# Kernel tuning notes

Measured on AMD Instinct MI355X. Metric: run time of the kernel, lower is better.

## Reference

```python
import jax, jax.numpy as jnp
import numpy as np

DEPTH = 3
N = 32768          # total nodes
G = 256            # num graphs
P = N // G         # nodes per graph (last node is the virtual node)
E = 524288         # edges
IN, H, H2 = 8, 64, 128


def _lin(key, out_d, in_d):
    w = jax.random.normal(key, (out_d, in_d), dtype=jnp.float32) * (1.0 / np.sqrt(in_d))
    b = jnp.zeros((out_d,), dtype=jnp.float32)
    return w, b


def setup_inputs() -> dict:
    key = jax.random.key(0)
    ks = jax.random.split(key, 10)
    x = jax.random.normal(ks[0], (N, IN), dtype=jnp.float32)
    edge_index = jax.random.randint(ks[1], (2, E), 0, N, dtype=jnp.int32).astype(jnp.int64)
    batch = (jnp.arange(N, dtype=jnp.int64) // P)
    W1, b1 = _lin(ks[2], H, IN)
    W2, b2 = _lin(ks[3], H, H)
    W3, b3 = _lin(ks[4], H, H)
    W4, b4 = _lin(ks[5], H, 2 * H)
    W5, b5 = _lin(ks[6], H, H * H)
    Wd1, bd1 = _lin(ks[7], H2, H)
    Wd2, bd2 = _lin(ks[8], 1, H2)
    return {"x": x, "edge_index": edge_index, "batch": batch, "num_graphs": G,
            "W1": W1, "b1": b1, "W2": W2, "b2": b2, "W3": W3, "b3": b3,
            "W4": W4, "b4": b4, "W5": W5, "b5": b5,
            "Wd1": Wd1, "bd1": bd1, "Wd2": Wd2, "bd2": bd2}


def reference(x, edge_index, batch, num_graphs,
              W1, b1, W2, b2, W3, b3, W4, b4, W5, b5, Wd1, bd1, Wd2, bd2):
    # initial embed: linear -> relu -> L2 normalize
    h = jax.nn.relu(x @ W1.T + b1)
    h = h / jnp.linalg.norm(h, axis=-1, keepdims=True)
    src, dst = edge_index[0], edge_index[1]
    for _ in range(DEPTH):
        # sum-aggregate neighbor messages (PyG add aggregation: gather src, scatter-add to dst)
        m = jax.ops.segment_sum(h[src], dst, num_segments=N)
        cat = jnp.concatenate([m @ W3.T + b3, h @ W2.T + b2], axis=-1)  # [N, 2H]
        h = jax.nn.relu(cat @ W4.T + b4)
        h = h / jnp.linalg.norm(h, axis=-1, keepdims=True)
    # per-graph: outer product of each non-virtual node embedding with the
    # last (virtual) node embedding. Graphs are equal-sized -> vectorize by reshape.
    hg = h.reshape(num_graphs, P, H)
    others = hg[:, :-1, :]          # [G, P-1, H]
    last = hg[:, -1, :]             # [G, H]
    outer = jnp.einsum('gpi,gj->gpij', others, last)        # [G, P-1, H, H]
    outer = outer.reshape(num_graphs * (P - 1), H * H)       # flatten(start_dim=1), row-major i*H+j
    y = outer @ W5.T + b5
    y = jax.nn.relu(y @ Wd1.T + bd1)
    y = y @ Wd2.T + bd2              # [G*(P-1), 1] Q-values
    return y
```

## Files before the change

kernel.cpp:

```cpp
#include <hip/hip_runtime.h>
#include <hip/hip_bf16.h>

#define NN 32768
#define EE 524288
#define GG 256
#define PP 128

__global__ void k_weights(const float* __restrict__ W2, const float* __restrict__ b2,
                          const float* __restrict__ W3, const float* __restrict__ b3,
                          const float* __restrict__ W4, const float* __restrict__ b4,
                          const float* __restrict__ Wd1, float* __restrict__ Wc,
                          float* __restrict__ Wd1t) {
    __shared__ float tile[128 * 65];
    int t = threadIdx.x;
    if (blockIdx.x == 32) {
        for (int idx = t; idx < 8192; idx += 256) {
            int q = idx >> 6, o = idx & 63;
            tile[q*65 + o] = Wd1[idx];
        }
        __syncthreads();
        for (int idx = t; idx < 8192; idx += 256) {
            int o = idx >> 7, q = idx & 127;
            Wd1t[idx] = tile[q*65 + o];
        }
        return;
    }
    int idx = blockIdx.x * 256 + t;
    int kk = idx >> 6, o = idx & 63;
    float a = 0.f;
    if (kk < 64) {
        for (int j = 0; j < 64; ++j) a += W4[o*128 + j] * W3[j*64 + kk];
    } else {
        int k2 = kk - 64;
        for (int j = 0; j < 64; ++j) a += W4[o*128 + 64 + j] * W2[j*64 + k2];
    }
    Wc[kk*64 + o] = a;
    if (idx < 64) {
        float c = b4[idx];
        for (int j = 0; j < 64; ++j)
            c += W4[idx*128 + j]*b3[j] + W4[idx*128 + 64 + j]*b2[j];
        Wc[8192 + idx] = c;
    }
}

__global__ void k_init(const float* __restrict__ x, const float* __restrict__ W1,
                       const float* __restrict__ b1, float* __restrict__ h,
                       int* __restrict__ deg) {
    if (blockIdx.x < 128) deg[blockIdx.x * 256 + threadIdx.x] = 0;
    int node = (blockIdx.x * blockDim.x + threadIdx.x) >> 6;
    int lane = threadIdx.x & 63;
    if (node >= NN) return;
    float acc = b1[lane];
    #pragma unroll
    for (int j = 0; j < 8; ++j)
        acc += x[node*8 + j] * W1[lane*8 + j];
    acc = fmaxf(acc, 0.f);
    float ss = acc * acc;
    #pragma unroll
    for (int m = 1; m < 64; m <<= 1) ss += __shfl_xor(ss, m, 64);
    h[node*64 + lane] = acc / sqrtf(ss);
}

__global__ void k_hist(const int* __restrict__ dst, int* __restrict__ deg) {
    int i = blockIdx.x * blockDim.x + threadIdx.x;
    int4 d = ((const int4*)dst)[i];
    atomicAdd(&deg[d.x], 1);
    atomicAdd(&deg[d.y], 1);
    atomicAdd(&deg[d.z], 1);
    atomicAdd(&deg[d.w], 1);
}

__global__ void __launch_bounds__(1024) k_scan(
        const int* __restrict__ deg, int* __restrict__ offs,
        int* __restrict__ cur) {
    __shared__ int part[1024];
    int t = threadIdx.x;
    int4 v[8];
    int base4 = t * 8;
    int s = 0;
    #pragma unroll
    for (int j = 0; j < 8; ++j) {
        v[j] = ((const int4*)deg)[base4 + j];
        s += v[j].x + v[j].y + v[j].z + v[j].w;
    }
    part[t] = s;
    __syncthreads();
    for (int off = 1; off < 1024; off <<= 1) {
        int tmp = (t >= off) ? part[t - off] : 0;
        __syncthreads();
        part[t] += tmp;
        __syncthreads();
    }
    int run = part[t] - s;
    #pragma unroll
    for (int j = 0; j < 8; ++j) {
        int4 o;
        o.x = run; run += v[j].x;
        o.y = run; run += v[j].y;
        o.z = run; run += v[j].z;
        o.w = run; run += v[j].w;
        ((int4*)offs)[base4 + j] = o;
        ((int4*)cur)[base4 + j]  = o;
    }
    if (t == 1023) offs[NN] = part[1023];
}

__global__ void k_fill(const int* __restrict__ src, const int* __restrict__ dst,
                       int* __restrict__ cur, int* __restrict__ csr) {
    int i = blockIdx.x * blockDim.x + threadIdx.x;
    int4 s4 = ((const int4*)src)[i];
    int4 d4 = ((const int4*)dst)[i];
    csr[atomicAdd(&cur[d4.x], 1)] = s4.x;
    csr[atomicAdd(&cur[d4.y], 1)] = s4.y;
    csr[atomicAdd(&cur[d4.z], 1)] = s4.z;
    csr[atomicAdd(&cur[d4.w], 1)] = s4.w;
}

__global__ void __launch_bounds__(256) k_gather(
        const float* __restrict__ h, const int* __restrict__ offs,
        const int* __restrict__ csr, float* __restrict__ m) {
    int node = (blockIdx.x * blockDim.x + threadIdx.x) >> 6;
    int lane = threadIdx.x & 63;
    int fg4 = (lane & 15) * 4, es = lane >> 4;
    int st = offs[node], de = offs[node + 1] - st;
    float4 acc = make_float4(0.f, 0.f, 0.f, 0.f);
    for (int e = es; e < de; e += 16) {
        int a0 = st + e;
        int a1 = min(st + e + 4,  EE - 1);
        int a2 = min(st + e + 8,  EE - 1);
        int a3 = min(st + e + 12, EE - 1);
        int i0 = csr[a0], i1 = csr[a1], i2 = csr[a2], i3 = csr[a3];
        float w1 = (e + 4  < de) ? 1.f : 0.f;
        float w2 = (e + 8  < de) ? 1.f : 0.f;
        float w3 = (e + 12 < de) ? 1.f : 0.f;
        float4 v0 = *(const float4*)&h[(long)i0*64 + fg4];
        float4 v1 = *(const float4*)&h[(long)i1*64 + fg4];
        float4 v2 = *(const float4*)&h[(long)i2*64 + fg4];
        float4 v3 = *(const float4*)&h[(long)i3*64 + fg4];
        acc.x += v0.x + w1*v1.x + w2*v2.x + w3*v3.x;
        acc.y += v0.y + w1*v1.y + w2*v2.y + w3*v3.y;
        acc.z += v0.z + w1*v1.z + w2*v2.z + w3*v3.z;
        acc.w += v0.w + w1*v1.w + w2*v2.w + w3*v3.w;
    }
    acc.x += __shfl_xor(acc.x, 16, 64); acc.y += __shfl_xor(acc.y, 16, 64);
    acc.z += __shfl_xor(acc.z, 16, 64); acc.w += __shfl_xor(acc.w, 16, 64);
    acc.x += __shfl_xor(acc.x, 32, 64); acc.y += __shfl_xor(acc.y, 32, 64);
    acc.z += __shfl_xor(acc.z, 32, 64); acc.w += __shfl_xor(acc.w, 32, 64);
    if (es == 0) *(float4*)&m[(long)node*64 + fg4] = acc;
}

__global__ void __launch_bounds__(256) k_gemm(
        const float* __restrict__ Wc, float* mio,
        const float* __restrict__ hcur) {
    __shared__ float Wl[8192];
    __shared__ float Xl[32 * 132];
    int t = threadIdx.x;
    int nbase = blockIdx.x * 32;

    for (int i = t * 4; i < 8192; i += 1024)
        *(float4*)&Wl[i] = *(const float4*)&Wc[i];
    for (int idx = t; idx < 512; idx += 256) {
        int n = idx >> 4, c = (idx & 15) * 4;
        *(float4*)&Xl[n*132 + c]      = *(const float4*)&mio[(long)(nbase+n)*64 + c];
        *(float4*)&Xl[n*132 + 64 + c] = *(const float4*)&hcur[(long)(nbase+n)*64 + c];
    }
    __syncthreads();

    int tc = t & 15, tr = t >> 4;
    int o0 = tc * 4, n0 = tr * 2;
    float4 c4 = *(const float4*)&Wc[8192 + o0];
    float acc0[4] = {0.f,0.f,0.f,0.f};
    float acc1[4] = {0.f,0.f,0.f,0.f};
    #pragma unroll 4
    for (int kk = 0; kk < 128; kk += 4) {
        float4 w0 = *(float4*)&Wl[(kk+0)*64 + o0];
        float4 w1 = *(float4*)&Wl[(kk+1)*64 + o0];
        float4 w2 = *(float4*)&Wl[(kk+2)*64 + o0];
        float4 w3 = *(float4*)&Wl[(kk+3)*64 + o0];
        float4 x0 = *(float4*)&Xl[(n0+0)*132 + kk];
        float4 x1 = *(float4*)&Xl[(n0+1)*132 + kk];
        acc0[0] += x0.x*w0.x + x0.y*w1.x + x0.z*w2.x + x0.w*w3.x;
        acc0[1] += x0.x*w0.y + x0.y*w1.y + x0.z*w2.y + x0.w*w3.y;
        acc0[2] += x0.x*w0.z + x0.y*w1.z + x0.z*w2.z + x0.w*w3.z;
        acc0[3] += x0.x*w0.w + x0.y*w1.w + x0.z*w2.w + x0.w*w3.w;
        acc1[0] += x1.x*w0.x + x1.y*w1.x + x1.z*w2.x + x1.w*w3.x;
        acc1[1] += x1.x*w0.y + x1.y*w1.y + x1.z*w2.y + x1.w*w3.y;
        acc1[2] += x1.x*w0.z + x1.y*w1.z + x1.z*w2.z + x1.w*w3.z;
        acc1[3] += x1.x*w0.w + x1.y*w1.w + x1.z*w2.w + x1.w*w3.w;
    }

    #pragma unroll
    for (int jn = 0; jn < 2; ++jn) {
        float* a = jn ? acc1 : acc0;
        float v0 = fmaxf(a[0] + c4.x, 0.f);
        float v1 = fmaxf(a[1] + c4.y, 0.f);
        float v2 = fmaxf(a[2] + c4.z, 0.f);
        float v3 = fmaxf(a[3] + c4.w, 0.f);
        float ss = v0*v0 + v1*v1 + v2*v2 + v3*v3;
        ss += __shfl_xor(ss, 1, 64);
        ss += __shfl_xor(ss, 2, 64);
        ss += __shfl_xor(ss, 4, 64);
        ss += __shfl_xor(ss, 8, 64);
        float r = 1.0f / sqrtf(ss);
        float4 outv = make_float4(v0*r, v1*r, v2*r, v3*r);
        *(float4*)&mio[(long)(nbase + n0 + jn)*64 + o0] = outv;
    }
}

__global__ void __launch_bounds__(256) k_tmat(
        const float* __restrict__ h, const float* __restrict__ W5,
        float* __restrict__ Tt) {
    __shared__ float lastL[256 * 65];
    __shared__ float wL[64 * 16];
    __shared__ float tr[16 * 257];
    int t = threadIdx.x;
    int rb = blockIdx.x * 16;
    int i = rb >> 6, obase = rb & 63;

    for (int idx4 = t; idx4 < 4096; idx4 += 256) {
        int g = idx4 >> 4, c = (idx4 & 15) * 4;
        *(float4*)&lastL[g*65 + c] =
            *(const float4*)&h[((long)g*128 + 127)*64 + c];
    }
    {
        int rr = t & 15, j0 = (t >> 4) * 4;
        float4 w = *(const float4*)&W5[(long)(obase + rr)*4096 + i*64 + j0];
        wL[(j0+0)*16 + rr] = w.x;
        wL[(j0+1)*16 + rr] = w.y;
        wL[(j0+2)*16 + rr] = w.z;
        wL[(j0+3)*16 + rr] = w.w;
    }
    __syncthreads();

    int g = t;
    float acc[16] = {};
    for (int j = 0; j < 64; ++j) {
        float lv = lastL[g*65 + j];
        #pragma unroll
        for (int r4 = 0; r4 < 4; ++r4) {
            float4 wv = *(float4*)&wL[j*16 + r4*4];
            acc[r4*4+0] += wv.x * lv;
            acc[r4*4+1] += wv.y * lv;
            acc[r4*4+2] += wv.z * lv;
            acc[r4*4+3] += wv.w * lv;
        }
    }
    #pragma unroll
    for (int rr = 0; rr < 16; ++rr) tr[rr*257 + g] = acc[rr];
    __syncthreads();
    for (int it = 0; it < 4; ++it) {
        int idx = t + it*256;
        int g2 = idx >> 2, c4 = idx & 3;
        float4 v = make_float4(tr[(c4*4+0)*257 + g2], tr[(c4*4+1)*257 + g2],
                               tr[(c4*4+2)*257 + g2], tr[(c4*4+3)*257 + g2]);
        *(float4*)&Tt[(long)g2*4096 + rb + c4*4] = v;
    }
}

__global__ void __launch_bounds__(256) k_readout(
        const float* __restrict__ h, const float* __restrict__ Tt,
        const float* __restrict__ b5, const float* __restrict__ Wd1t,
        const float* __restrict__ bd1, const float* __restrict__ Wd2,
        const float* __restrict__ bd2, float* __restrict__ out) {
    __shared__ float Tl[4096];
    __shared__ float W1t[8192];
    __shared__ float OY[32 * 68];
    int t = threadIdx.x;
    int g = blockIdx.x >> 1, half = blockIdx.x & 1;

    for (int i = t * 4; i < 4096; i += 1024)
        *(float4*)&Tl[i] = *(const float4*)&Tt[(long)g*4096 + i];
    for (int i = t * 4; i < 8192; i += 1024)
        *(float4*)&W1t[i] = *(const float4*)&Wd1t[i];

    int tc = t & 15, tr = t >> 4;
    int o0 = tc * 4, p0 = tr * 2;
    int tc2 = t & 31, tr2 = t >> 5;
    int q0 = tc2 * 4, pp0 = tr2 * 4;
    float4 b5_4  = *(const float4*)&b5[o0];
    float4 bd1_4 = *(const float4*)&bd1[q0];
    float4 wd2_4 = *(const float4*)&Wd2[q0];
    float bd2v = bd2[0];

    for (int pt = half*2; pt < half*2 + 2; ++pt) {
        int pbase = pt * 32;
        __syncthreads();
        for (int idx = t; idx < 512; idx += 256) {
            int p = idx >> 4, c = (idx & 15) * 4;
            *(float4*)&OY[p*68 + c] =
                *(const float4*)&h[((long)g*128 + pbase + p)*64 + c];
        }
        __syncthreads();

        float a10[4] = {0.f,0.f,0.f,0.f};
        float a11[4] = {0.f,0.f,0.f,0.f};
        #pragma unroll 4
        for (int i = 0; i < 64; i += 4) {
            float4 w0 = *(float4*)&Tl[(i+0)*64 + o0];
            float4 w1 = *(float4*)&Tl[(i+1)*64 + o0];
            float4 w2 = *(float4*)&Tl[(i+2)*64 + o0];
            float4 w3 = *(float4*)&Tl[(i+3)*64 + o0];
            float4 x0 = *(float4*)&OY[(p0+0)*68 + i];
            float4 x1 = *(float4*)&OY[(p0+1)*68 + i];
            a10[0] += x0.x*w0.x + x0.y*w1.x + x0.z*w2.x + x0.w*w3.x;
            a10[1] += x0.x*w0.y + x0.y*w1.y + x0.z*w2.y + x0.w*w3.y;
            a10[2] += x0.x*w0.z + x0.y*w1.z + x0.z*w2.z + x0.w*w3.z;
            a10[3] += x0.x*w0.w + x0.y*w1.w + x0.z*w2.w + x0.w*w3.w;
            a11[0] += x1.x*w0.x + x1.y*w1.x + x1.z*w2.x + x1.w*w3.x;
            a11[1] += x1.x*w0.y + x1.y*w1.y + x1.z*w2.y + x1.w*w3.y;
            a11[2] += x1.x*w0.z + x1.y*w1.z + x1.z*w2.z + x1.w*w3.z;
            a11[3] += x1.x*w0.w + x1.y*w1.w + x1.z*w2.w + x1.w*w3.w;
        }
        __syncthreads();

        float4 y0 = make_float4(a10[0]+b5_4.x, a10[1]+b5_4.y, a10[2]+b5_4.z, a10[3]+b5_4.w);
        float4 y1 = make_float4(a11[0]+b5_4.x, a11[1]+b5_4.y, a11[2]+b5_4.z, a11[3]+b5_4.w);
        *(float4*)&OY[(p0+0)*68 + o0] = y0;
        *(float4*)&OY[(p0+1)*68 + o0] = y1;
        __syncthreads();

        float a2[4][4] = {};
        #pragma unroll 4
        for (int o = 0; o < 64; o += 4) {
            float4 w0 = *(float4*)&W1t[(o+0)*128 + q0];
            float4 w1 = *(float4*)&W1t[(o+1)*128 + q0];
            float4 w2 = *(float4*)&W1t[(o+2)*128 + q0];
            float4 w3 = *(float4*)&W1t[(o+3)*128 + q0];
            #pragma unroll
            for (int jp = 0; jp < 4; ++jp) {
                float4 yv = *(float4*)&OY[(pp0+jp)*68 + o];
                a2[jp][0] += yv.x*w0.x + yv.y*w1.x + yv.z*w2.x + yv.w*w3.x;
                a2[jp][1] += yv.x*w0.y + yv.y*w1.y + yv.z*w2.y + yv.w*w3.y;
                a2[jp][2] += yv.x*w0.z + yv.y*w1.z + yv.z*w2.z + yv.w*w3.z;
                a2[jp][3] += yv.x*w0.w + yv.y*w1.w + yv.z*w2.w + yv.w*w3.w;
            }
        }

        #pragma unroll
        for (int jp = 0; jp < 4; ++jp) {
            float s = wd2_4.x * fmaxf(a2[jp][0] + bd1_4.x, 0.f)
                    + wd2_4.y * fmaxf(a2[jp][1] + bd1_4.y, 0.f)
                    + wd2_4.z * fmaxf(a2[jp][2] + bd1_4.z, 0.f)
                    + wd2_4.w * fmaxf(a2[jp][3] + bd1_4.w, 0.f);
            s += __shfl_xor(s, 1, 64);
            s += __shfl_xor(s, 2, 64);
            s += __shfl_xor(s, 4, 64);
            s += __shfl_xor(s, 8, 64);
            s += __shfl_xor(s, 16, 64);
            if (tc2 == 0) {
                int p = pbase + pp0 + jp;
                if (p < 127) out[g*127 + p] = s + bd2v;
            }
        }
    }
}

extern "C" void kernel_launch(void* const* d_in, const int* in_sizes, int n_in,
                              void* d_out, int out_size, void* d_ws, size_t ws_size,
                              hipStream_t stream) {
    const float* x   = (const float*)d_in[0];
    const int*   ei  = (const int*)d_in[1];
    const float* W1  = (const float*)d_in[4];
    const float* b1  = (const float*)d_in[5];
    const float* W2  = (const float*)d_in[6];
    const float* b2  = (const float*)d_in[7];
    const float* W3  = (const float*)d_in[8];
    const float* b3  = (const float*)d_in[9];
    const float* W4  = (const float*)d_in[10];
    const float* b4  = (const float*)d_in[11];
    const float* W5  = (const float*)d_in[12];
    const float* b5  = (const float*)d_in[13];
    const float* Wd1 = (const float*)d_in[14];
    const float* bd1 = (const float*)d_in[15];
    const float* Wd2 = (const float*)d_in[16];
    const float* bd2 = (const float*)d_in[17];
    float* out = (float*)d_out;

    float* ws  = (float*)d_ws;
    float* h0   = ws;
    float* h1   = ws + 2097152;
    float* Tt   = ws + 4194304;
    float* Wc   = ws + 5242880;
    float* Wd1t = ws + 5251328;
    int*   deg  = (int*)(ws + 5259520);
    int*   offs = deg + NN;
    int*   cur  = offs + NN + 16;
    int*   csr  = cur + NN;

    const int* src = ei;
    const int* dst = ei + EE;

    k_weights<<<33, 256, 0, stream>>>(W2, b2, W3, b3, W4, b4, Wd1, Wc, Wd1t);
    k_init<<<NN/4, 256, 0, stream>>>(x, W1, b1, h0, deg);

    k_hist<<<EE/1024, 256, 0, stream>>>(dst, deg);
    k_scan<<<1, 1024, 0, stream>>>(deg, offs, cur);
    k_fill<<<EE/1024, 256, 0, stream>>>(src, dst, cur, csr);

    float* hc = h0; float* hn = h1;
    for (int l = 0; l < 3; ++l) {
        k_gather<<<NN/4, 256, 0, stream>>>(hc, offs, csr, hn);
        k_gemm<<<NN/32, 256, 0, stream>>>(Wc, hn, hc);
        float* tmp = hc; hc = hn; hn = tmp;
    }

    k_tmat<<<256, 256, 0, stream>>>(hc, W5, Tt);
    k_readout<<<512, 256, 0, stream>>>(hc, Tt, b5, Wd1t, bd1, Wd2, bd2, out);
}
```

Before: 306.7 us.

## Pad CSR rows to multiples of four, fuse weight prep into init, widen GEMM tile

Each CSR segment is padded to a multiple of four entries. Padding slots point to an extra zero row appended to the h buffers, so the gather loads an int4 of neighbor indices and sums four rows with no masks or clamps. The weight-precompute kernel is merged into the init kernel to save a launch. The GEMM tile grows from 32 to 64 nodes per block, with each thread computing four rows instead of two. This adds a CSR prefill pass and more register and LDS use per block in the GEMM.

```diff
diff --git a/kernel.cpp b/kernel.cpp
--- a/kernel.cpp
+++ b/kernel.cpp
@@ -5,51 +5,56 @@
 #define EE 524288
 #define GG 256
 #define PP 128
-
-__global__ void k_weights(const float* __restrict__ W2, const float* __restrict__ b2,
-                          const float* __restrict__ W3, const float* __restrict__ b3,
-                          const float* __restrict__ W4, const float* __restrict__ b4,
-                          const float* __restrict__ Wd1, float* __restrict__ Wc,
-                          float* __restrict__ Wd1t) {
+#define CSR_CAP4 155652
+
+__global__ void k_init(const float* __restrict__ x, const float* __restrict__ W1,
+                       const float* __restrict__ b1,
+                       const float* __restrict__ W2, const float* __restrict__ b2,
+                       const float* __restrict__ W3, const float* __restrict__ b3,
+                       const float* __restrict__ W4, const float* __restrict__ b4,
+                       const float* __restrict__ Wd1,
+                       float* __restrict__ h0, float* __restrict__ h1,
+                       float* __restrict__ Wc, float* __restrict__ Wd1t,
+                       int* __restrict__ deg) {
     __shared__ float tile[128 * 65];
-    int t = threadIdx.x;
-    if (blockIdx.x == 32) {
-        for (int idx = t; idx < 8192; idx += 256) {
-            int q = idx >> 6, o = idx & 63;
-            tile[q*65 + o] = Wd1[idx];
-        }
-        __syncthreads();
-        for (int idx = t; idx < 8192; idx += 256) {
-            int o = idx >> 7, q = idx & 127;
-            Wd1t[idx] = tile[q*65 + o];
+    int b = blockIdx.x, t = threadIdx.x;
+    if (b >= 8192) {
+        if (b == 8224) {
+            for (int idx = t; idx < 8192; idx += 256) {
+                int q = idx >> 6, o = idx & 63;
+                tile[q*65 + o] = Wd1[idx];
+            }
+            __syncthreads();
+            for (int idx = t; idx < 8192; idx += 256) {
+                int o = idx >> 7, q = idx & 127;
+                Wd1t[idx] = tile[q*65 + o];
+            }
+        } else if (b == 8225) {
+            if (t < 64)       h0[(long)NN*64 + t] = 0.f;
+            else if (t < 128) h1[(long)NN*64 + (t-64)] = 0.f;
+        } else {
+            int idx = (b - 8192) * 256 + t;
+            int kk = idx >> 6, o = idx & 63;
+            float a = 0.f;
+            if (kk < 64) {
+                for (int j = 0; j < 64; ++j) a += W4[o*128 + j] * W3[j*64 + kk];
+            } else {
+                int k2 = kk - 64;
+                for (int j = 0; j < 64; ++j) a += W4[o*128 + 64 + j] * W2[j*64 + k2];
+            }
+            Wc[kk*64 + o] = a;
+            if (idx < 64) {
+                float c = b4[idx];
+                for (int j = 0; j < 64; ++j)
+                    c += W4[idx*128 + j]*b3[j] + W4[idx*128 + 64 + j]*b2[j];
+                Wc[8192 + idx] = c;
+            }
         }
         return;
     }
-    int idx = blockIdx.x * 256 + t;
-    int kk = idx >> 6, o = idx & 63;
-    float a = 0.f;
-    if (kk < 64) {
-        for (int j = 0; j < 64; ++j) a += W4[o*128 + j] * W3[j*64 + kk];
-    } else {
-        int k2 = kk - 64;
-        for (int j = 0; j < 64; ++j) a += W4[o*128 + 64 + j] * W2[j*64 + k2];
-    }
-    Wc[kk*64 + o] = a;
-    if (idx < 64) {
-        float c = b4[idx];
-        for (int j = 0; j < 64; ++j)
-            c += W4[idx*128 + j]*b3[j] + W4[idx*128 + 64 + j]*b2[j];
-        Wc[8192 + idx] = c;
-    }
-}
-
-__global__ void k_init(const float* __restrict__ x, const float* __restrict__ W1,
-                       const float* __restrict__ b1, float* __restrict__ h,
-                       int* __restrict__ deg) {
-    if (blockIdx.x < 128) deg[blockIdx.x * 256 + threadIdx.x] = 0;
-    int node = (blockIdx.x * blockDim.x + threadIdx.x) >> 6;
-    int lane = threadIdx.x & 63;
-    if (node >= NN) return;
+    if (b < 128) deg[b * 256 + t] = 0;
+    int node = (b * 256 + t) >> 6;
+    int lane = t & 63;
     float acc = b1[lane];
     #pragma unroll
     for (int j = 0; j < 8; ++j)
@@ -58,16 +63,20 @@
     float ss = acc * acc;
     #pragma unroll
     for (int m = 1; m < 64; m <<= 1) ss += __shfl_xor(ss, m, 64);
-    h[node*64 + lane] = acc / sqrtf(ss);
-}
-
-__global__ void k_hist(const int* __restrict__ dst, int* __restrict__ deg) {
+    h0[node*64 + lane] = acc / sqrtf(ss);
+}
+
+__global__ void k_hist(const int* __restrict__ dst, int* __restrict__ deg,
+                       int* __restrict__ csr) {
     int i = blockIdx.x * blockDim.x + threadIdx.x;
     int4 d = ((const int4*)dst)[i];
     atomicAdd(&deg[d.x], 1);
     atomicAdd(&deg[d.y], 1);
     atomicAdd(&deg[d.z], 1);
     atomicAdd(&deg[d.w], 1);
+    int4 s = make_int4(NN, NN, NN, NN);
+    for (int j = i; j < CSR_CAP4; j += 131072)
+        ((int4*)csr)[j] = s;
 }
 
 __global__ void __launch_bounds__(1024) k_scan(
@@ -81,7 +90,7 @@
     #pragma unroll
     for (int j = 0; j < 8; ++j) {
         v[j] = ((const int4*)deg)[base4 + j];
-        s += v[j].x + v[j].y + v[j].z + v[j].w;
+        s += ((v[j].x+3)&~3) + ((v[j].y+3)&~3) + ((v[j].z+3)&~3) + ((v[j].w+3)&~3);
     }
     part[t] = s;
     __syncthreads();
@@ -95,10 +104,10 @@
     #pragma unroll
     for (int j = 0; j < 8; ++j) {
         int4 o;
-        o.x = run; run += v[j].x;
-        o.y = run; run += v[j].y;
-        o.z = run; run += v[j].z;
-        o.w = run; run += v[j].w;
+        o.x = run; run += (v[j].x+3)&~3;
+        o.y = run; run += (v[j].y+3)&~3;
+        o.z = run; run += (v[j].z+3)&~3;
+        o.w = run; run += (v[j].w+3)&~3;
         ((int4*)offs)[base4 + j] = o;
         ((int4*)cur)[base4 + j]  = o;
     }
@@ -122,25 +131,21 @@
     int node = (blockIdx.x * blockDim.x + threadIdx.x) >> 6;
     int lane = threadIdx.x & 63;
     int fg4 = (lane & 15) * 4, es = lane >> 4;
-    int st = offs[node], de = offs[node + 1] - st;
+    int st = offs[node];
+    int de4 = (offs[node + 1] - st) >> 2;
+    int st4 = st >> 2;
+    const int4* csr4 = (const int4*)csr;
     float4 acc = make_float4(0.f, 0.f, 0.f, 0.f);
-    for (int e = es; e < de; e += 16) {
-        int a0 = st + e;
-        int a1 = min(st + e + 4,  EE - 1);
-        int a2 = min(st + e + 8,  EE - 1);
-        int a3 = min(st + e + 12, EE - 1);
-        int i0 = csr[a0], i1 = csr[a1], i2 = csr[a2], i3 = csr[a3];
-        float w1 = (e + 4  < de) ? 1.f : 0.f;
-        float w2 = (e + 8  < de) ? 1.f : 0.f;
-        float w3 = (e + 12 < de) ? 1.f : 0.f;
-        float4 v0 = *(const float4*)&h[(long)i0*64 + fg4];
-        float4 v1 = *(const float4*)&h[(long)i1*64 + fg4];
-        float4 v2 = *(const float4*)&h[(long)i2*64 + fg4];
-        float4 v3 = *(const float4*)&h[(long)i3*64 + fg4];
-        acc.x += v0.x + w1*v1.x + w2*v2.x + w3*v3.x;
-        acc.y += v0.y + w1*v1.y + w2*v2.y + w3*v3.y;
-        acc.z += v0.z + w1*v1.z + w2*v2.z + w3*v3.z;
-        acc.w += v0.w + w1*v1.w + w2*v2.w + w3*v3.w;
+    for (int q = es; q < de4; q += 4) {
+        int4 idx = csr4[st4 + q];
+        float4 v0 = *(const float4*)&h[(long)idx.x*64 + fg4];
+        float4 v1 = *(const float4*)&h[(long)idx.y*64 + fg4];
+        float4 v2 = *(const float4*)&h[(long)idx.z*64 + fg4];
+        float4 v3 = *(const float4*)&h[(long)idx.w*64 + fg4];
+        acc.x += (v0.x + v1.x) + (v2.x + v3.x);
+        acc.y += (v0.y + v1.y) + (v2.y + v3.y);
+        acc.z += (v0.z + v1.z) + (v2.z + v3.z);
+        acc.w += (v0.w + v1.w) + (v2.w + v3.w);
     }
     acc.x += __shfl_xor(acc.x, 16, 64); acc.y += __shfl_xor(acc.y, 16, 64);
     acc.z += __shfl_xor(acc.z, 16, 64); acc.w += __shfl_xor(acc.w, 16, 64);
@@ -153,13 +158,13 @@
         const float* __restrict__ Wc, float* mio,
         const float* __restrict__ hcur) {
     __shared__ float Wl[8192];
-    __shared__ float Xl[32 * 132];
+    __shared__ float Xl[64 * 132];
     int t = threadIdx.x;
-    int nbase = blockIdx.x * 32;
+    int nbase = blockIdx.x * 64;
 
     for (int i = t * 4; i < 8192; i += 1024)
         *(float4*)&Wl[i] = *(const float4*)&Wc[i];
-    for (int idx = t; idx < 512; idx += 256) {
+    for (int idx = t; idx < 1024; idx += 256) {
         int n = idx >> 4, c = (idx & 15) * 4;
         *(float4*)&Xl[n*132 + c]      = *(const float4*)&mio[(long)(nbase+n)*64 + c];
         *(float4*)&Xl[n*132 + 64 + c] = *(const float4*)&hcur[(long)(nbase+n)*64 + c];
@@ -167,35 +172,31 @@
     __syncthreads();
 
     int tc = t & 15, tr = t >> 4;
-    int o0 = tc * 4, n0 = tr * 2;
+    int o0 = tc * 4, n0 = tr * 4;
     float4 c4 = *(const float4*)&Wc[8192 + o0];
-    float acc0[4] = {0.f,0.f,0.f,0.f};
-    float acc1[4] = {0.f,0.f,0.f,0.f};
-    #pragma unroll 4
+    float acc[4][4] = {};
+    #pragma unroll 2
     for (int kk = 0; kk < 128; kk += 4) {
         float4 w0 = *(float4*)&Wl[(kk+0)*64 + o0];
         float4 w1 = *(float4*)&Wl[(kk+1)*64 + o0];
         float4 w2 = *(float4*)&Wl[(kk+2)*64 + o0];
         float4 w3 = *(float4*)&Wl[(kk+3)*64 + o0];
-        float4 x0 = *(float4*)&Xl[(n0+0)*132 + kk];
-        float4 x1 = *(float4*)&Xl[(n0+1)*132 + kk];
-        acc0[0] += x0.x*w0.x + x0.y*w1.x + x0.z*w2.x + x0.w*w3.x;
-        acc0[1] += x0.x*w0.y + x0.y*w1.y + x0.z*w2.y + x0.w*w3.y;
-        acc0[2] += x0.x*w0.z + x0.y*w1.z + x0.z*w2.z + x0.w*w3.z;
-        acc0[3] += x0.x*w0.w + x0.y*w1.w + x0.z*w2.w + x0.w*w3.w;
-        acc1[0] += x1.x*w0.x + x1.y*w1.x + x1.z*w2.x + x1.w*w3.x;
-        acc1[1] += x1.x*w0.y + x1.y*w1.y + x1.z*w2.y + x1.w*w3.y;
-        acc1[2] += x1.x*w0.z + x1.y*w1.z + x1.z*w2.z + x1.w*w3.z;
-        acc1[3] += x1.x*w0.w + x1.y*w1.w + x1.z*w2.w + x1.w*w3.w;
-    }
-
-    #pragma unroll
-    for (int jn = 0; jn < 2; ++jn) {
-        float* a = jn ? acc1 : acc0;
-        float v0 = fmaxf(a[0] + c4.x, 0.f);
-        float v1 = fmaxf(a[1] + c4.y, 0.f);
-        float v2 = fmaxf(a[2] + c4.z, 0.f);
-        float v3 = fmaxf(a[3] + c4.w, 0.f);
+        #pragma unroll
+        for (int jn = 0; jn < 4; ++jn) {
+            float4 xv = *(float4*)&Xl[(n0+jn)*132 + kk];
+            acc[jn][0] += xv.x*w0.x + xv.y*w1.x + xv.z*w2.x + xv.w*w3.x;
+            acc[jn][1] += xv.x*w0.y + xv.y*w1.y + xv.z*w2.y + xv.w*w3.y;
+            acc[jn][2] += xv.x*w0.z + xv.y*w1.z + xv.z*w2.z + xv.w*w3.z;
+            acc[jn][3] += xv.x*w0.w + xv.y*w1.w + xv.z*w2.w + xv.w*w3.w;
+        }
+    }
+
+    #pragma unroll
+    for (int jn = 0; jn < 4; ++jn) {
+        float v0 = fmaxf(acc[jn][0] + c4.x, 0.f);
+        float v1 = fmaxf(acc[jn][1] + c4.y, 0.f);
+        float v2 = fmaxf(acc[jn][2] + c4.z, 0.f);
+        float v3 = fmaxf(acc[jn][3] + c4.w, 0.f);
         float ss = v0*v0 + v1*v1 + v2*v2 + v3*v3;
         ss += __shfl_xor(ss, 1, 64);
         ss += __shfl_xor(ss, 2, 64);
@@ -378,11 +379,11 @@
 
     float* ws  = (float*)d_ws;
     float* h0   = ws;
-    float* h1   = ws + 2097152;
-    float* Tt   = ws + 4194304;
-    float* Wc   = ws + 5242880;
-    float* Wd1t = ws + 5251328;
-    int*   deg  = (int*)(ws + 5259520);
+    float* h1   = ws + 2129984;
+    float* Tt   = ws + 4259968;
+    float* Wc   = ws + 5308416;
+    float* Wd1t = ws + 5316864;
+    int*   deg  = (int*)(ws + 5325056);
     int*   offs = deg + NN;
     int*   cur  = offs + NN + 16;
     int*   csr  = cur + NN;
@@ -390,17 +391,16 @@
     const int* src = ei;
     const int* dst = ei + EE;
 
-    k_weights<<<33, 256, 0, stream>>>(W2, b2, W3, b3, W4, b4, Wd1, Wc, Wd1t);
-    k_init<<<NN/4, 256, 0, stream>>>(x, W1, b1, h0, deg);
-
-    k_hist<<<EE/1024, 256, 0, stream>>>(dst, deg);
+    k_init<<<8226, 256, 0, stream>>>(x, W1, b1, W2, b2, W3, b3, W4, b4,
+                                     Wd1, h0, h1, Wc, Wd1t, deg);
+    k_hist<<<512, 256, 0, stream>>>(dst, deg, csr);
     k_scan<<<1, 1024, 0, stream>>>(deg, offs, cur);
-    k_fill<<<EE/1024, 256, 0, stream>>>(src, dst, cur, csr);
+    k_fill<<<512, 256, 0, stream>>>(src, dst, cur, csr);
 
     float* hc = h0; float* hn = h1;
     for (int l = 0; l < 3; ++l) {
         k_gather<<<NN/4, 256, 0, stream>>>(hc, offs, csr, hn);
-        k_gemm<<<NN/32, 256, 0, stream>>>(Wc, hn, hc);
+        k_gemm<<<NN/64, 256, 0, stream>>>(Wc, hn, hc);
         float* tmp = hc; hc = hn; hn = tmp;
     }
 
```

Result: no change. 308.4 us (+0.5%).
